# Performance work log

Measured on AMD Instinct MI355X. Metric: run time of the kernel, lower is better.

Reference implementation:

```python
import jax, jax.numpy as jnp
import numpy as np

BLOCK = 8
WIN = 3
PAD = WIN - 1


def _dct_mat(b, dtype):
    # Orthonormal DCT-II matrix: D[k, n] = s_k * sqrt(2/b) * cos(pi*(2n+1)k/(2b))
    n = np.arange(b)
    k = n[:, None]
    D = np.sqrt(2.0 / b) * np.cos(np.pi * (2 * n[None, :] + 1) * k / (2 * b))
    D[0, :] *= 1.0 / np.sqrt(2.0)
    return jnp.asarray(D, dtype=dtype)


def setup_inputs() -> dict:
    key = jax.random.key(0)
    k1, k2 = jax.random.split(key)
    x = jax.random.normal(k1, (8, 64, 256, 256), dtype=jnp.float32)
    conv_w = jax.random.normal(k2, (64, 64, WIN), dtype=jnp.float32) * 0.05
    conv_b = jnp.zeros((64,), dtype=jnp.float32)
    return {"x": x, "conv_w": conv_w, "conv_b": conv_b}


def reference(x, conv_w, conv_b):
    b = BLOCK
    bsz, ch, H, W = x.shape
    nH, nW = H // b, W // b
    n = nH * nW
    D = _dct_mat(b, x.dtype)

    # blockify: (bsz, ch, n_blocks, b, b)
    blk = x.reshape(bsz, ch, nH, b, nW, b).transpose(0, 1, 2, 4, 3, 5)
    blk = blk.reshape(bsz, ch, n, b, b)

    # block 2D DCT: D @ X @ D^T
    coef = jnp.einsum('kn,bcxnm,lm->bcxkl', D, blk, D)
    coef = coef.reshape(bsz, ch, n, b * b)

    # FreqConv: causal-right-padded Conv1d over the b*b frequency axis
    y = coef.transpose(0, 2, 1, 3).reshape(bsz * n, ch, b * b)
    y = jnp.pad(y, ((0, 0), (0, 0), (0, PAD)))
    y = jax.lax.conv_general_dilated(
        y, conv_w, window_strides=(1,), padding=[(0, 0)],
        dimension_numbers=('NCH', 'OIH', 'NCH'), feature_group_count=1)
    y = y + conv_b[None, :, None]
    out_ch = y.shape[1]
    y = y.reshape(bsz, n, out_ch, b * b).transpose(0, 2, 1, 3)

    # block 2D IDCT: D^T @ X @ D
    y = y.reshape(bsz, out_ch, n, b, b)
    img = jnp.einsum('kn,bcxkl,lm->bcxnm', D, y, D)

    # deblockify back to (bsz, out_ch, H, W)
    img = img.reshape(bsz, out_ch, nH, nW, b, b).transpose(0, 1, 2, 4, 3, 5)
    return img.reshape(bsz, out_ch, H, W)
```

## Files before the change

kernel.cpp:

```cpp
#include <hip/hip_runtime.h>


#define THREADS 256
#define HW 256
#define CH 64
#define CT_ROW 72
#define CT_SAMPLE (66 * CT_ROW)
#define LDS_BYTES (4 * CT_SAMPLE * 2)

typedef __attribute__((ext_vector_type(8))) short short8b;
typedef __attribute__((ext_vector_type(4))) float f32x4;
typedef __attribute__((ext_vector_type(4))) unsigned short us4;
typedef __attribute__((ext_vector_type(8))) unsigned short us8;

__device__ inline unsigned short f2bf(float f) {
    unsigned u = __builtin_bit_cast(unsigned, f);
    u += 0x7FFFu + ((u >> 16) & 1u);
    return (unsigned short)(u >> 16);
}
__device__ inline float bf2f(unsigned short h) {
    unsigned u = ((unsigned)h) << 16;
    return __builtin_bit_cast(float, u);
}

__device__ __constant__ static const float D8[8][8] = {
  { 0.3535533906f, 0.3535533906f, 0.3535533906f, 0.3535533906f, 0.3535533906f, 0.3535533906f, 0.3535533906f, 0.3535533906f },
  { 0.4903926402f, 0.4157348062f, 0.2777851165f, 0.0975451610f,-0.0975451610f,-0.2777851165f,-0.4157348062f,-0.4903926402f },
  { 0.4619397663f, 0.1913417162f,-0.1913417162f,-0.4619397663f,-0.4619397663f,-0.1913417162f, 0.1913417162f, 0.4619397663f },
  { 0.4157348062f,-0.0975451610f,-0.4903926402f,-0.2777851165f, 0.2777851165f, 0.4903926402f, 0.0975451610f,-0.4157348062f },
  { 0.3535533906f,-0.3535533906f,-0.3535533906f, 0.3535533906f, 0.3535533906f,-0.3535533906f,-0.3535533906f, 0.3535533906f },
  { 0.2777851165f,-0.4903926402f, 0.0975451610f, 0.4157348062f,-0.4157348062f,-0.0975451610f, 0.4903926402f,-0.2777851165f },
  { 0.1913417162f,-0.4619397663f, 0.4619397663f,-0.1913417162f,-0.1913417162f, 0.4619397663f,-0.4619397663f, 0.1913417162f },
  { 0.0975451610f,-0.2777851165f, 0.4157348062f,-0.4903926402f, 0.4903926402f,-0.4157348062f, 0.2777851165f,-0.0975451610f },
};

__global__ __launch_bounds__(256)
void wt_prep_kernel(const float* __restrict__ conv_w, unsigned short* __restrict__ wt) {
    int j = blockIdx.x * 256 + threadIdx.x;
    int w = j >> 12;
    int rem = j & 4095;
    int o = rem >> 6;
    int i = rem & 63;
    wt[j] = f2bf(conv_w[o * 192 + i * 3 + w]);
}

__global__ __launch_bounds__(THREADS, 4)
void dct_freq_conv_kernel(const float* __restrict__ x,
                          const unsigned short* __restrict__ wt,
                          const float* __restrict__ conv_b,
                          float* __restrict__ out)
{
    extern __shared__ char smem[];
    unsigned short* Ct = (unsigned short*)smem;

    const int tid = threadIdx.x;
    const int bz  = blockIdx.z;
    const int by  = blockIdx.y;
    const int bx0 = blockIdx.x * 4;

    const int c   = tid >> 2;
    const int blk = tid & 3;

    {
        int s = tid >> 6, i = tid & 63;
        Ct[s * CT_SAMPLE + 64 * CT_ROW + i] = 0;
        Ct[s * CT_SAMPLE + 65 * CT_ROW + i] = 0;
    }

    {
        const float* xp = x + ((((size_t)bz * CH + c) * HW + by * 8) * HW
                               + (bx0 + blk) * 8);
        float v[8][8];
        #pragma unroll
        for (int r = 0; r < 8; ++r) {
            float4 a = *reinterpret_cast<const float4*>(xp + r * HW);
            float4 b = *reinterpret_cast<const float4*>(xp + r * HW + 4);
            v[r][0] = a.x; v[r][1] = a.y; v[r][2] = a.z; v[r][3] = a.w;
            v[r][4] = b.x; v[r][5] = b.y; v[r][6] = b.z; v[r][7] = b.w;
        }
        #pragma unroll
        for (int n = 0; n < 8; ++n) {
            float r[8];
            #pragma unroll
            for (int l = 0; l < 8; ++l) {
                float s = 0.f;
                #pragma unroll
                for (int m = 0; m < 8; ++m) s = fmaf(v[n][m], D8[l][m], s);
                r[l] = s;
            }
            #pragma unroll
            for (int l = 0; l < 8; ++l) v[n][l] = r[l];
        }
        unsigned short* ctw = Ct + blk * CT_SAMPLE + c;
        #pragma unroll
        for (int l = 0; l < 8; ++l) {
            #pragma unroll
            for (int k = 0; k < 8; ++k) {
                float s = 0.f;
                #pragma unroll
                for (int n = 0; n < 8; ++n) s = fmaf(D8[k][n], v[n][l], s);
                ctw[(k * 8 + l) * CT_ROW] = f2bf(s);
            }
        }
    }

    __syncthreads();

    const int wid  = tid >> 6;
    const int lane = tid & 63;
    const int lr   = lane & 15;
    const int lq   = lane >> 4;

    f32x4 acc[4][4];
    #pragma unroll
    for (int n = 0; n < 4; ++n)
        #pragma unroll
        for (int m = 0; m < 4; ++m)
            acc[n][m] = (f32x4){0.f, 0.f, 0.f, 0.f};

    unsigned short* CtP = Ct + wid * CT_SAMPLE;

    #pragma unroll
    for (int kc = 0; kc < 6; ++kc) {
        const int w  = kc >> 1;
        const int i0 = (kc & 1) * 32 + 8 * lq;
        short8b a[4], b[4];
        #pragma unroll
        for (int n = 0; n < 4; ++n)
            a[n] = *(const short8b*)&CtP[(n * 16 + lr + w) * CT_ROW + i0];
        #pragma unroll
        for (int m = 0; m < 4; ++m)
            b[m] = *(const short8b*)&wt[(w * 64 + m * 16 + lr) * 64 + i0];
        #pragma unroll
        for (int n = 0; n < 4; ++n)
            #pragma unroll
            for (int m = 0; m < 4; ++m)
                acc[n][m] = __builtin_amdgcn_mfma_f32_16x16x32_bf16(
                    a[n], b[m], acc[n][m], 0, 0, 0);
    }

    #pragma unroll
    for (int n = 0; n < 4; ++n) {
        const int t0 = n * 16 + 4 * lq;
        #pragma unroll
        for (int m = 0; m < 4; ++m) {
            const int o = m * 16 + lr;
            us4 pk;
            #pragma unroll
            for (int j = 0; j < 4; ++j) pk[j] = f2bf(acc[n][m][j]);
            *(us4*)&CtP[o * CT_ROW + t0] = pk;
        }
    }

    __syncthreads();

    {
        const unsigned short* yb = Ct + blk * CT_SAMPLE + c * CT_ROW;
        const float bias = conv_b[c];
        float y[64];
        #pragma unroll
        for (int j = 0; j < 8; ++j) {
            us8 v = *(const us8*)&yb[j * 8];
            #pragma unroll
            for (int e = 0; e < 8; ++e) y[j * 8 + e] = bf2f(v[e]) + bias;
        }
        #pragma unroll
        for (int l = 0; l < 8; ++l) {
            float r[8];
            #pragma unroll
            for (int n = 0; n < 8; ++n) {
                float s = 0.f;
                #pragma unroll
                for (int k = 0; k < 8; ++k) s = fmaf(D8[k][n], y[k * 8 + l], s);
                r[n] = s;
            }
            #pragma unroll
            for (int n = 0; n < 8; ++n) y[n * 8 + l] = r[n];
        }
        float* op = out + ((((size_t)bz * CH + c) * HW + by * 8) * HW
                           + (bx0 + blk) * 8);
        #pragma unroll
        for (int n = 0; n < 8; ++n) {
            float o8[8];
            #pragma unroll
            for (int m = 0; m < 8; ++m) {
                float s = 0.f;
                #pragma unroll
                for (int l = 0; l < 8; ++l) s = fmaf(y[n * 8 + l], D8[l][m], s);
                o8[m] = s;
            }
            *reinterpret_cast<float4*>(op + n * HW)     = make_float4(o8[0], o8[1], o8[2], o8[3]);
            *reinterpret_cast<float4*>(op + n * HW + 4) = make_float4(o8[4], o8[5], o8[6], o8[7]);
        }
    }
}

extern "C" void kernel_launch(void* const* d_in, const int* in_sizes, int n_in,
                              void* d_out, int out_size, void* d_ws, size_t ws_size,
                              hipStream_t stream) {
    const float* x  = (const float*)d_in[0];
    const float* cw = (const float*)d_in[1];
    const float* cb = (const float*)d_in[2];
    float* o        = (float*)d_out;
    unsigned short* wtb = (unsigned short*)d_ws;

    wt_prep_kernel<<<dim3(48), dim3(256), 0, stream>>>(cw, wtb);

    hipFuncSetAttribute(reinterpret_cast<const void*>(dct_freq_conv_kernel),
                        hipFuncAttributeMaxDynamicSharedMemorySize,
                        (int)LDS_BYTES);
    dim3 grid(8, 32, 8);
    dct_freq_conv_kernel<<<grid, dim3(THREADS), LDS_BYTES, stream>>>(x, wtb, cb, o);
}
```

Baseline: 266.2 us.

## Compute block DCT and IDCT as Kronecker-matrix MFMA GEMMs per wavefront

```diff
diff --git a/kernel.cpp b/kernel.cpp
--- a/kernel.cpp
+++ b/kernel.cpp
@@ -9,18 +9,14 @@
 #define LDS_BYTES (4 * CT_SAMPLE * 2)
 
 typedef __attribute__((ext_vector_type(8))) short short8b;
+typedef __attribute__((ext_vector_type(8))) unsigned short us8;
 typedef __attribute__((ext_vector_type(4))) float f32x4;
 typedef __attribute__((ext_vector_type(4))) unsigned short us4;
-typedef __attribute__((ext_vector_type(8))) unsigned short us8;
 
 __device__ inline unsigned short f2bf(float f) {
     unsigned u = __builtin_bit_cast(unsigned, f);
     u += 0x7FFFu + ((u >> 16) & 1u);
     return (unsigned short)(u >> 16);
-}
-__device__ inline float bf2f(unsigned short h) {
-    unsigned u = ((unsigned)h) << 16;
-    return __builtin_bit_cast(float, u);
 }
 
 __device__ __constant__ static const float D8[8][8] = {
@@ -35,92 +31,104 @@
 };
 
 __global__ __launch_bounds__(256)
-void wt_prep_kernel(const float* __restrict__ conv_w, unsigned short* __restrict__ wt) {
+void prep_kernel(const float* __restrict__ conv_w, unsigned short* __restrict__ ws16) {
     int j = blockIdx.x * 256 + threadIdx.x;
-    int w = j >> 12;
-    int rem = j & 4095;
-    int o = rem >> 6;
-    int i = rem & 63;
-    wt[j] = f2bf(conv_w[o * 192 + i * 3 + w]);
+    if (j < 4096) {
+        int t = j >> 6, s = j & 63;
+        ws16[j] = f2bf(D8[t >> 3][s >> 3] * D8[t & 7][s & 7]);
+    } else if (j < 8192) {
+        int jj = j - 4096;
+        int s = jj >> 6, t = jj & 63;
+        ws16[j] = f2bf(D8[t >> 3][s >> 3] * D8[t & 7][s & 7]);
+    } else if (j < 20480) {
+        int jj = j - 8192;
+        int w = jj >> 12, rem = jj & 4095, o = rem >> 6, i = rem & 63;
+        ws16[j] = f2bf(conv_w[o * 192 + i * 3 + w]);
+    }
 }
 
 __global__ __launch_bounds__(THREADS, 4)
 void dct_freq_conv_kernel(const float* __restrict__ x,
-                          const unsigned short* __restrict__ wt,
+                          const unsigned short* __restrict__ ws16,
                           const float* __restrict__ conv_b,
                           float* __restrict__ out)
 {
     extern __shared__ char smem[];
     unsigned short* Ct = (unsigned short*)smem;
-
-    const int tid = threadIdx.x;
-    const int bz  = blockIdx.z;
-    const int by  = blockIdx.y;
-    const int bx0 = blockIdx.x * 4;
-
-    const int c   = tid >> 2;
-    const int blk = tid & 3;
-
-    {
-        int s = tid >> 6, i = tid & 63;
-        Ct[s * CT_SAMPLE + 64 * CT_ROW + i] = 0;
-        Ct[s * CT_SAMPLE + 65 * CT_ROW + i] = 0;
-    }
-
-    {
-        const float* xp = x + ((((size_t)bz * CH + c) * HW + by * 8) * HW
-                               + (bx0 + blk) * 8);
-        float v[8][8];
-        #pragma unroll
-        for (int r = 0; r < 8; ++r) {
-            float4 a = *reinterpret_cast<const float4*>(xp + r * HW);
-            float4 b = *reinterpret_cast<const float4*>(xp + r * HW + 4);
-            v[r][0] = a.x; v[r][1] = a.y; v[r][2] = a.z; v[r][3] = a.w;
-            v[r][4] = b.x; v[r][5] = b.y; v[r][6] = b.z; v[r][7] = b.w;
-        }
-        #pragma unroll
-        for (int n = 0; n < 8; ++n) {
-            float r[8];
-            #pragma unroll
-            for (int l = 0; l < 8; ++l) {
-                float s = 0.f;
-                #pragma unroll
-                for (int m = 0; m < 8; ++m) s = fmaf(v[n][m], D8[l][m], s);
-                r[l] = s;
-            }
-            #pragma unroll
-            for (int l = 0; l < 8; ++l) v[n][l] = r[l];
-        }
-        unsigned short* ctw = Ct + blk * CT_SAMPLE + c;
-        #pragma unroll
-        for (int l = 0; l < 8; ++l) {
-            #pragma unroll
-            for (int k = 0; k < 8; ++k) {
-                float s = 0.f;
-                #pragma unroll
-                for (int n = 0; n < 8; ++n) s = fmaf(D8[k][n], v[n][l], s);
-                ctw[(k * 8 + l) * CT_ROW] = f2bf(s);
-            }
-        }
-    }
-
-    __syncthreads();
-
+    const unsigned short* Trm = ws16;
+    const unsigned short* Urm = ws16 + 4096;
+    const unsigned short* Wt  = ws16 + 8192;
+
+    const int tid  = threadIdx.x;
     const int wid  = tid >> 6;
     const int lane = tid & 63;
     const int lr   = lane & 15;
     const int lq   = lane >> 4;
-
-    f32x4 acc[4][4];
+    const int bz   = blockIdx.z;
+    const int by   = blockIdx.y;
+    const int bxs  = blockIdx.x * 4 + wid;
+
+    unsigned short* CtP = Ct + wid * CT_SAMPLE;
+
+    if (lane < 36) *(us4*)&CtP[64 * CT_ROW + lane * 4] = (us4){0, 0, 0, 0};
+
+    float bias[4];
+    #pragma unroll
+    for (int m = 0; m < 4; ++m) bias[m] = conv_b[m * 16 + lr];
+
+    #pragma unroll
+    for (int mg = 0; mg < 2; ++mg) {
+        f32x4 acc[2][4];
+        #pragma unroll
+        for (int i = 0; i < 2; ++i)
+            #pragma unroll
+            for (int n = 0; n < 4; ++n) acc[i][n] = (f32x4){0.f, 0.f, 0.f, 0.f};
+
+        #pragma unroll
+        for (int kc = 0; kc < 2; ++kc) {
+            short8b a[2], b[4];
+            #pragma unroll
+            for (int mh = 0; mh < 2; ++mh) {
+                const int c = (mg * 2 + mh) * 16 + lr;
+                const float* xp = x + (((size_t)bz * CH + c) * HW + by * 8 + kc * 4 + lq) * HW
+                                    + bxs * 8;
+                float4 u0 = *(const float4*)xp;
+                float4 u1 = *(const float4*)(xp + 4);
+                us8 pa;
+                pa[0] = f2bf(u0.x); pa[1] = f2bf(u0.y); pa[2] = f2bf(u0.z); pa[3] = f2bf(u0.w);
+                pa[4] = f2bf(u1.x); pa[5] = f2bf(u1.y); pa[6] = f2bf(u1.z); pa[7] = f2bf(u1.w);
+                a[mh] = __builtin_bit_cast(short8b, pa);
+            }
+            #pragma unroll
+            for (int n = 0; n < 4; ++n)
+                b[n] = *(const short8b*)&Trm[(n * 16 + lr) * 64 + kc * 32 + lq * 8];
+            #pragma unroll
+            for (int mh = 0; mh < 2; ++mh)
+                #pragma unroll
+                for (int n = 0; n < 4; ++n)
+                    acc[mh][n] = __builtin_amdgcn_mfma_f32_16x16x32_bf16(
+                        a[mh], b[n], acc[mh][n], 0, 0, 0);
+        }
+        #pragma unroll
+        for (int mh = 0; mh < 2; ++mh) {
+            const int c0 = (mg * 2 + mh) * 16 + lq * 4;
+            #pragma unroll
+            for (int n = 0; n < 4; ++n) {
+                us4 pk;
+                #pragma unroll
+                for (int j = 0; j < 4; ++j) pk[j] = f2bf(acc[mh][n][j]);
+                *(us4*)&CtP[(n * 16 + lr) * CT_ROW + c0] = pk;
+            }
+        }
+    }
+
+    f32x4 acc2[4][4];
     #pragma unroll
     for (int n = 0; n < 4; ++n)
         #pragma unroll
-        for (int m = 0; m < 4; ++m)
-            acc[n][m] = (f32x4){0.f, 0.f, 0.f, 0.f};
-
-    unsigned short* CtP = Ct + wid * CT_SAMPLE;
-
-    #pragma unroll
+        for (int m = 0; m < 4; ++m) acc2[n][m] = (f32x4){0.f, 0.f, 0.f, 0.f};
+
+    #pragma unroll 2
     for (int kc = 0; kc < 6; ++kc) {
         const int w  = kc >> 1;
         const int i0 = (kc & 1) * 32 + 8 * lq;
@@ -130,15 +138,14 @@
             a[n] = *(const short8b*)&CtP[(n * 16 + lr + w) * CT_ROW + i0];
         #pragma unroll
         for (int m = 0; m < 4; ++m)
-            b[m] = *(const short8b*)&wt[(w * 64 + m * 16 + lr) * 64 + i0];
+            b[m] = *(const short8b*)&Wt[(w * 64 + m * 16 + lr) * 64 + i0];
         #pragma unroll
         for (int n = 0; n < 4; ++n)
             #pragma unroll
             for (int m = 0; m < 4; ++m)
-                acc[n][m] = __builtin_amdgcn_mfma_f32_16x16x32_bf16(
-                    a[n], b[m], acc[n][m], 0, 0, 0);
-    }
-
+                acc2[n][m] = __builtin_amdgcn_mfma_f32_16x16x32_bf16(
+                    a[n], b[m], acc2[n][m], 0, 0, 0);
+    }
     #pragma unroll
     for (int n = 0; n < 4; ++n) {
         const int t0 = n * 16 + 4 * lq;
@@ -147,50 +154,48 @@
             const int o = m * 16 + lr;
             us4 pk;
             #pragma unroll
-            for (int j = 0; j < 4; ++j) pk[j] = f2bf(acc[n][m][j]);
+            for (int j = 0; j < 4; ++j) pk[j] = f2bf(acc2[n][m][j] + bias[m]);
             *(us4*)&CtP[o * CT_ROW + t0] = pk;
         }
     }
 
-    __syncthreads();
-
-    {
-        const unsigned short* yb = Ct + blk * CT_SAMPLE + c * CT_ROW;
-        const float bias = conv_b[c];
-        float y[64];
-        #pragma unroll
-        for (int j = 0; j < 8; ++j) {
-            us8 v = *(const us8*)&yb[j * 8];
-            #pragma unroll
-            for (int e = 0; e < 8; ++e) y[j * 8 + e] = bf2f(v[e]) + bias;
-        }
-        #pragma unroll
-        for (int l = 0; l < 8; ++l) {
-            float r[8];
-            #pragma unroll
-            for (int n = 0; n < 8; ++n) {
-                float s = 0.f;
+    #pragma unroll
+    for (int mg = 0; mg < 2; ++mg) {
+        f32x4 acc[2][4];
+        #pragma unroll
+        for (int i = 0; i < 2; ++i)
+            #pragma unroll
+            for (int ct = 0; ct < 4; ++ct) acc[i][ct] = (f32x4){0.f, 0.f, 0.f, 0.f};
+
+        #pragma unroll
+        for (int kc = 0; kc < 2; ++kc) {
+            short8b a[2], b[4];
+            #pragma unroll
+            for (int mh = 0; mh < 2; ++mh)
+                a[mh] = *(const short8b*)&Urm[((mg * 2 + mh) * 16 + lr) * 64 + kc * 32 + lq * 8];
+            #pragma unroll
+            for (int ct = 0; ct < 4; ++ct)
+                b[ct] = *(const short8b*)&CtP[(ct * 16 + lr) * CT_ROW + kc * 32 + lq * 8];
+            #pragma unroll
+            for (int mh = 0; mh < 2; ++mh)
                 #pragma unroll
-                for (int k = 0; k < 8; ++k) s = fmaf(D8[k][n], y[k * 8 + l], s);
-                r[n] = s;
+                for (int ct = 0; ct < 4; ++ct)
+                    acc[mh][ct] = __builtin_amdgcn_mfma_f32_16x16x32_bf16(
+                        a[mh], b[ct], acc[mh][ct], 0, 0, 0);
+        }
+        #pragma unroll
+        for (int mh = 0; mh < 2; ++mh) {
+            const int s0 = (mg * 2 + mh) * 16 + lq * 4;
+            const int n  = s0 >> 3;
+            const int m0 = s0 & 7;
+            #pragma unroll
+            for (int ct = 0; ct < 4; ++ct) {
+                const int o = ct * 16 + lr;
+                float4 st = make_float4(acc[mh][ct][0], acc[mh][ct][1],
+                                        acc[mh][ct][2], acc[mh][ct][3]);
+                *(float4*)(out + (((size_t)bz * CH + o) * HW + by * 8 + n) * HW
+                           + bxs * 8 + m0) = st;
             }
-            #pragma unroll
-            for (int n = 0; n < 8; ++n) y[n * 8 + l] = r[n];
-        }
-        float* op = out + ((((size_t)bz * CH + c) * HW + by * 8) * HW
-                           + (bx0 + blk) * 8);
-        #pragma unroll
-        for (int n = 0; n < 8; ++n) {
-            float o8[8];
-            #pragma unroll
-            for (int m = 0; m < 8; ++m) {
-                float s = 0.f;
-                #pragma unroll
-                for (int l = 0; l < 8; ++l) s = fmaf(y[n * 8 + l], D8[l][m], s);
-                o8[m] = s;
-            }
-            *reinterpret_cast<float4*>(op + n * HW)     = make_float4(o8[0], o8[1], o8[2], o8[3]);
-            *reinterpret_cast<float4*>(op + n * HW + 4) = make_float4(o8[4], o8[5], o8[6], o8[7]);
         }
     }
 }
@@ -202,13 +207,13 @@
     const float* cw = (const float*)d_in[1];
     const float* cb = (const float*)d_in[2];
     float* o        = (float*)d_out;
-    unsigned short* wtb = (unsigned short*)d_ws;
-
-    wt_prep_kernel<<<dim3(48), dim3(256), 0, stream>>>(cw, wtb);
+    unsigned short* ws16 = (unsigned short*)d_ws;
+
+    prep_kernel<<<dim3(80), dim3(256), 0, stream>>>(cw, ws16);
 
     hipFuncSetAttribute(reinterpret_cast<const void*>(dct_freq_conv_kernel),
                         hipFuncAttributeMaxDynamicSharedMemorySize,
                         (int)LDS_BYTES);
     dim3 grid(8, 32, 8);
-    dct_freq_conv_kernel<<<grid, dim3(THREADS), LDS_BYTES, stream>>>(x, wtb, cb, o);
-}
+    dct_freq_conv_kernel<<<grid, dim3(THREADS), LDS_BYTES, stream>>>(x, ws16, cb, o);
+}
```

Result: slower. 286.0 us (+7.4%).
